# Kernel tuning notes

Measured on AMD Instinct MI355X. Metric: run time of the kernel, lower is better.

Reference implementation:

```python
import jax, jax.numpy as jnp
import numpy as np

N_NODES = 50000
IN_DIM = 128
OUT_DIM = 128
N_EDGES = 800000


def setup_inputs() -> dict:
    key = jax.random.key(0)
    k1, k2, k3, k4 = jax.random.split(key, 4)
    h = jax.random.normal(k1, (N_NODES, IN_DIM), dtype=jnp.float32)
    edges = jax.random.randint(k2, (2, N_EDGES), 0, N_NODES, dtype=jnp.int64)
    # nn.Linear params
    lim = 1.0 / np.sqrt(IN_DIM)
    W = jax.random.uniform(k3, (OUT_DIM, IN_DIM), minval=-lim, maxval=lim, dtype=jnp.float32)
    b = jax.random.uniform(k4, (OUT_DIM,), minval=-lim, maxval=lim, dtype=jnp.float32)
    return {"h": h, "W": W, "b": b, "edges": edges}


def reference(h, W, b, edges):
    n = h.shape[0]
    # add self loops (use_self_loops=True)
    loops = jnp.arange(n, dtype=edges.dtype)
    src = jnp.concatenate([edges[0], loops])  # [E+N]
    dst = jnp.concatenate([edges[1], loops])  # [E+N]
    # linear transform
    h_ = h @ W.T + b  # [N, out_dim]
    # symmetric normalization: 1/sqrt(deg(src)*deg(dst)), degrees incl. self loops
    deg = jax.ops.segment_sum(jnp.ones_like(dst, dtype=h.dtype), dst, num_segments=n)
    ew = jax.lax.rsqrt(deg[src] * deg[dst])  # [E+N]
    # edge-weighted scatter-sum aggregation
    agg = jax.ops.segment_sum(h_[src] * ew[:, None], dst, num_segments=n)
    return agg
```

## Files before the change

### kernel.cpp

```cpp
#include <hip/hip_runtime.h>


#define IN_DIM 128
#define OUT_DIM 128
#define CAP 40
#define NB_A 256
#define NBIN 784
#define BINW 64
#define CAPA 16
#define OVB 8
#define OVCAP 4096

typedef short bf16x8 __attribute__((ext_vector_type(8)));
typedef float f32x4 __attribute__((ext_vector_type(4)));
typedef unsigned short us8 __attribute__((ext_vector_type(8)));
typedef unsigned short us4 __attribute__((ext_vector_type(4)));

__device__ __forceinline__ unsigned short f2bf(float f) {
    unsigned u = __float_as_uint(f);
    u += 0x7fffu + ((u >> 16) & 1u);
    return (unsigned short)(u >> 16);
}
__device__ __forceinline__ float bf2f(unsigned short s) {
    return __uint_as_float(((unsigned)s) << 16);
}
__device__ __forceinline__ void accw(float4& acc, ushort4 v, float wt) {
    acc.x += wt * bf2f(v.x);
    acc.y += wt * bf2f(v.y);
    acc.z += wt * bf2f(v.z);
    acc.w += wt * bf2f(v.w);
}
__device__ __forceinline__ bf16x8 load_a8(const float* h, int row, int k0, int n) {
    bf16x8 r;
    if (row < n) {
        const float4* p = (const float4*)(h + (size_t)row * 128 + k0);
        float4 f0 = p[0], f1 = p[1];
        r[0] = (short)f2bf(f0.x); r[1] = (short)f2bf(f0.y);
        r[2] = (short)f2bf(f0.z); r[3] = (short)f2bf(f0.w);
        r[4] = (short)f2bf(f1.x); r[5] = (short)f2bf(f1.y);
        r[6] = (short)f2bf(f1.z); r[7] = (short)f2bf(f1.w);
    } else {
        r = (bf16x8){0, 0, 0, 0, 0, 0, 0, 0};
    }
    return r;
}

__global__ __launch_bounds__(256) void k_gb(
        const float* __restrict__ h, const float* __restrict__ W,
        const float* __restrict__ b, unsigned short* __restrict__ hsb, int n,
        const int* __restrict__ ed, unsigned* __restrict__ gbuf,
        int* __restrict__ gcnt, int* __restrict__ aovb, int2* __restrict__ aov,
        int* __restrict__ ctrs, int E, int ngemm) {
    __shared__ __align__(16) unsigned short sB[128 * 136];
    __shared__ int ovc;
    __shared__ int2 ovl[OVB];
    const int tid = threadIdx.x;

    if ((int)blockIdx.x >= ngemm) {
        int blk = blockIdx.x - ngemm;
        if (blk == 0 && tid == 0) ctrs[0] = 0;
        int* bc = (int*)sB;
        for (int i = tid; i < NBIN; i += 256) bc[i] = 0;
        if (tid == 0) ovc = 0;
        __syncthreads();
        const int chunk = (E + NB_A - 1) / NB_A;
        const int e0 = blk * chunk, e1 = min(E, e0 + chunk);
        for (int e = e0 + tid; e < e1; e += 256) {
            int s = ed[e];
            int d = ed[E + e];
            int bin = d >> 6, dlo = d & 63;
            int r = atomicAdd(&bc[bin], 1);
            if (r < CAPA) {
                gbuf[((size_t)blk * NBIN + bin) * CAPA + r] =
                    (unsigned)s | ((unsigned)dlo << 16);
            } else {
                int k = atomicAdd(&ovc, 1);
                if (k < OVB) ovl[k] = make_int2(s, d);
            }
        }
        __syncthreads();
        for (int i = tid; i < NBIN; i += 256)
            gcnt[(size_t)blk * NBIN + i] = min(bc[i], CAPA);
        int nov = min(ovc, OVB);
        if (tid < nov) aov[blk * OVB + tid] = ovl[tid];
        if (tid == 0) aovb[blk] = nov;
        return;
    }

    const int lane = tid & 63;
    const int wv = tid >> 6;
    const int quad = lane >> 4;
    const int l16 = lane & 15;
    const int row0 = blockIdx.x * 128;

    {
        const float4* W4 = (const float4*)W;
        for (int t = tid; t < 128 * 32; t += 256) {
            float4 w = W4[t];
            ushort4 q;
            q.x = f2bf(w.x); q.y = f2bf(w.y); q.z = f2bf(w.z); q.w = f2bf(w.w);
            ((ushort4*)sB)[(t >> 5) * 34 + (t & 31)] = q;
        }
    }
    __syncthreads();

    f32x4 acc[2][8];
#pragma unroll
    for (int mt = 0; mt < 2; ++mt)
#pragma unroll
        for (int nt = 0; nt < 8; ++nt) acc[mt][nt] = (f32x4){0.f, 0.f, 0.f, 0.f};

    const int koff = quad * 8;
    const int ra0 = row0 + wv * 32 + l16;
    const int ra1 = ra0 + 16;
#pragma unroll
    for (int kc = 0; kc < 4; ++kc) {
        int kbase = kc * 32 + koff;
        bf16x8 a0 = load_a8(h, ra0, kbase, n);
        bf16x8 a1 = load_a8(h, ra1, kbase, n);
#pragma unroll
        for (int nt = 0; nt < 8; ++nt) {
            bf16x8 bb = *(const bf16x8*)(sB + (nt * 16 + l16) * 136 + kbase);
            acc[0][nt] = __builtin_amdgcn_mfma_f32_16x16x32_bf16(a0, bb, acc[0][nt], 0, 0, 0);
            acc[1][nt] = __builtin_amdgcn_mfma_f32_16x16x32_bf16(a1, bb, acc[1][nt], 0, 0, 0);
        }
    }

#pragma unroll
    for (int mt = 0; mt < 2; ++mt) {
#pragma unroll
        for (int r = 0; r < 4; ++r) {
            int row = row0 + wv * 32 + mt * 16 + quad * 4 + r;
            if (row >= n) continue;
#pragma unroll
            for (int nt = 0; nt < 8; ++nt) {
                int col = nt * 16 + l16;
                hsb[(size_t)row * 128 + col] = f2bf(acc[mt][nt][r] + b[col]);
            }
        }
    }
}

__global__ __launch_bounds__(256) void k_binB(const unsigned* __restrict__ gbuf,
                                              const int* __restrict__ gcnt,
                                              const int* __restrict__ aovb,
                                              const int2* __restrict__ aov,
                                              unsigned short* __restrict__ ell,
                                              int* __restrict__ cnt,
                                              float* __restrict__ rs,
                                              int2* __restrict__ ovf2,
                                              int* __restrict__ ovf2c, int n) {
    __shared__ int lcnt[BINW];
    __shared__ __align__(16) unsigned short ells[BINW * CAP];
    const int tid = threadIdx.x;
    const int bin = blockIdx.x;
    const int node0 = bin * BINW;

    if (tid < BINW) lcnt[tid] = 0;
    __syncthreads();

    {
        int c = gcnt[(size_t)tid * NBIN + bin];
        const int4* cell4 = (const int4*)(gbuf + ((size_t)tid * NBIN + bin) * CAPA);
        int4 q0 = cell4[0];
        int4 q1 = cell4[1];
        int4 q2 = cell4[2];
        int4 q3 = cell4[3];
#define PROC(REC, J)                                              \
        if ((J) < c) {                                            \
            unsigned rec = (unsigned)(REC);                       \
            int src = rec & 0xffff;                               \
            int dlo = rec >> 16;                                  \
            int r = atomicAdd(&lcnt[dlo], 1);                     \
            if (r < CAP) {                                        \
                ells[dlo * CAP + r] = (unsigned short)src;        \
            } else {                                              \
                int k = atomicAdd(ovf2c, 1);                      \
                if (k < OVCAP) ovf2[k] = make_int2(src, node0 + dlo); \
            }                                                     \
        }
        PROC(q0.x, 0)  PROC(q0.y, 1)  PROC(q0.z, 2)  PROC(q0.w, 3)
        PROC(q1.x, 4)  PROC(q1.y, 5)  PROC(q1.z, 6)  PROC(q1.w, 7)
        PROC(q2.x, 8)  PROC(q2.y, 9)  PROC(q2.z, 10) PROC(q2.w, 11)
        PROC(q3.x, 12) PROC(q3.y, 13) PROC(q3.z, 14) PROC(q3.w, 15)
#undef PROC
    }
    {
        int cov = aovb[tid];
        for (int j = 0; j < cov; ++j) {
            int2 p = aov[tid * OVB + j];
            if ((p.y >> 6) == bin) {
                int dlo = p.y & 63;
                int r = atomicAdd(&lcnt[dlo], 1);
                if (r < CAP) {
                    ells[dlo * CAP + r] = (unsigned short)p.x;
                } else {
                    int k = atomicAdd(ovf2c, 1);
                    if (k < OVCAP) ovf2[k] = make_int2(p.x, node0 + dlo);
                }
            }
        }
    }
    __syncthreads();
    if (tid < BINW) {
        int node = node0 + tid;
        if (node < n) {
            cnt[node] = lcnt[tid];
            rs[node] = rsqrtf((float)(lcnt[tid] + 1));
        }
    }
    const int4* sp = (const int4*)ells;
    int4* dp = (int4*)(ell + (size_t)node0 * CAP);
#pragma unroll
    for (int i = tid; i < BINW * CAP * 2 / 16; i += 256) dp[i] = sp[i];
}

__global__ __launch_bounds__(256) void k_agg(const int* __restrict__ cnt,
                                             const float* __restrict__ rs,
                                             const unsigned short* __restrict__ ell,
                                             const int2* __restrict__ ovf2,
                                             const int* __restrict__ ovf2c,
                                             const unsigned short* __restrict__ hsb,
                                             float* __restrict__ out, int n) {
    int node = blockIdx.x * 8 + (threadIdx.x >> 5);
    if (node >= n) return;
    int lane = threadIdx.x & 31;
    int deg = cnt[node];
    float rsn = rs[node];
    int m = min(deg, CAP);

    const ushort4* hp = (const ushort4*)hsb;
    ushort4 sv = hp[(size_t)node * 32 + lane];
    float4 acc;
    acc.x = rsn * bf2f(sv.x); acc.y = rsn * bf2f(sv.y);
    acc.z = rsn * bf2f(sv.z); acc.w = rsn * bf2f(sv.w);

    const unsigned short* row = ell + (size_t)node * CAP;
    int e = 0;
    for (; e + 8 <= m; e += 8) {
        us8 p = *(const us8*)(row + e);
        float w0 = rs[p[0]], w1 = rs[p[1]], w2 = rs[p[2]], w3 = rs[p[3]];
        float w4 = rs[p[4]], w5 = rs[p[5]], w6 = rs[p[6]], w7 = rs[p[7]];
        ushort4 v0 = hp[(size_t)p[0] * 32 + lane];
        ushort4 v1 = hp[(size_t)p[1] * 32 + lane];
        ushort4 v2 = hp[(size_t)p[2] * 32 + lane];
        ushort4 v3 = hp[(size_t)p[3] * 32 + lane];
        ushort4 v4 = hp[(size_t)p[4] * 32 + lane];
        ushort4 v5 = hp[(size_t)p[5] * 32 + lane];
        ushort4 v6 = hp[(size_t)p[6] * 32 + lane];
        ushort4 v7 = hp[(size_t)p[7] * 32 + lane];
        accw(acc, v0, w0); accw(acc, v1, w1); accw(acc, v2, w2); accw(acc, v3, w3);
        accw(acc, v4, w4); accw(acc, v5, w5); accw(acc, v6, w6); accw(acc, v7, w7);
    }
    if (e + 4 <= m) {
        us4 p = *(const us4*)(row + e);
        float w0 = rs[p[0]], w1 = rs[p[1]], w2 = rs[p[2]], w3 = rs[p[3]];
        ushort4 v0 = hp[(size_t)p[0] * 32 + lane];
        ushort4 v1 = hp[(size_t)p[1] * 32 + lane];
        ushort4 v2 = hp[(size_t)p[2] * 32 + lane];
        ushort4 v3 = hp[(size_t)p[3] * 32 + lane];
        accw(acc, v0, w0); accw(acc, v1, w1); accw(acc, v2, w2); accw(acc, v3, w3);
        e += 4;
    }
    for (; e < m; ++e) {
        int s = row[e];
        accw(acc, hp[(size_t)s * 32 + lane], rs[s]);
    }
    if (deg > CAP) {
        int novf = min(*ovf2c, OVCAP);
        for (int i = 0; i < novf; ++i) {
            int2 p = ovf2[i];
            if (p.y == node) {
                accw(acc, hp[(size_t)p.x * 32 + lane], rs[p.x]);
            }
        }
    }
    acc.x *= rsn; acc.y *= rsn; acc.z *= rsn; acc.w *= rsn;
    ((float4*)out)[(size_t)node * 32 + lane] = acc;
}

extern "C" void kernel_launch(void* const* d_in, const int* in_sizes, int n_in,
                              void* d_out, int out_size, void* d_ws, size_t ws_size,
                              hipStream_t stream) {
    const float* h = (const float*)d_in[0];
    const float* W = (const float*)d_in[1];
    const float* b = (const float*)d_in[2];
    const int* edges = (const int*)d_in[3];

    const int n = in_sizes[0] / IN_DIM;
    const int E = in_sizes[3] / 2;
    const int ngemm = (n + 127) / 128;
    const int nnode_pad = NBIN * BINW;

    size_t o = 0;
    auto carve = [&](size_t elems) {
        size_t cur = o;
        o += (elems + 511) & ~(size_t)511;
        return cur;
    };
    float* ws = (float*)d_ws;
    unsigned short* hsb = (unsigned short*)(ws + carve((size_t)n * 64));
    unsigned* gbuf = (unsigned*)(ws + carve((size_t)NB_A * NBIN * CAPA));
    int* gcnt = (int*)(ws + carve((size_t)NB_A * NBIN));
    int* aovb = (int*)(ws + carve(NB_A));
    int2* aov = (int2*)(ws + carve((size_t)NB_A * OVB * 2));
    int* cnt = (int*)(ws + carve(nnode_pad));
    float* rs = ws + carve(nnode_pad);
    unsigned short* ell = (unsigned short*)(ws + carve((size_t)nnode_pad * CAP / 2));
    int2* ovf2 = (int2*)(ws + carve(OVCAP * 2));
    int* ctrs = (int*)(ws + carve(2));

    float* out = (float*)d_out;

    k_gb<<<ngemm + NB_A, 256, 0, stream>>>(h, W, b, hsb, n, edges, gbuf, gcnt,
                                           aovb, aov, ctrs, E, ngemm);
    k_binB<<<NBIN, 256, 0, stream>>>(gbuf, gcnt, aovb, aov, ell, cnt, rs,
                                     ovf2, ctrs, n);
    k_agg<<<(n + 7) / 8, 256, 0, stream>>>(cnt, rs, ell, ovf2, ctrs, hsb, out, n);
}
```

Baseline: 138.5 us.

## Split fused GEMM/binning kernel into separate launches with LDS-staged A tiles

Separates the combined edge-binning and linear-transform kernel into two kernels, k_binA and k_gemm, so the binning blocks no longer share the GEMM kernel's large LDS allocation and grid. The GEMM now uses 64-row tiles and stages the h rows into shared memory as bf16 before the MFMA loop, instead of each wave loading and converting its A fragments straight from global memory. This adds an extra kernel launch and removes the concurrency between binning and GEMM that the fused launch provided. It also doubles the number of GEMM blocks, each of which redundantly converts the full W matrix.

Result: slower. 142.3 us (+2.7%).

```diff
diff --git a/kernel.cpp b/kernel.cpp
--- a/kernel.cpp
+++ b/kernel.cpp
@@ -30,71 +30,70 @@
     acc.z += wt * bf2f(v.z);
     acc.w += wt * bf2f(v.w);
 }
-__device__ __forceinline__ bf16x8 load_a8(const float* h, int row, int k0, int n) {
-    bf16x8 r;
-    if (row < n) {
-        const float4* p = (const float4*)(h + (size_t)row * 128 + k0);
-        float4 f0 = p[0], f1 = p[1];
-        r[0] = (short)f2bf(f0.x); r[1] = (short)f2bf(f0.y);
-        r[2] = (short)f2bf(f0.z); r[3] = (short)f2bf(f0.w);
-        r[4] = (short)f2bf(f1.x); r[5] = (short)f2bf(f1.y);
-        r[6] = (short)f2bf(f1.z); r[7] = (short)f2bf(f1.w);
-    } else {
-        r = (bf16x8){0, 0, 0, 0, 0, 0, 0, 0};
-    }
-    return r;
-}
-
-__global__ __launch_bounds__(256) void k_gb(
-        const float* __restrict__ h, const float* __restrict__ W,
-        const float* __restrict__ b, unsigned short* __restrict__ hsb, int n,
-        const int* __restrict__ ed, unsigned* __restrict__ gbuf,
-        int* __restrict__ gcnt, int* __restrict__ aovb, int2* __restrict__ aov,
-        int* __restrict__ ctrs, int E, int ngemm) {
-    __shared__ __align__(16) unsigned short sB[128 * 136];
+
+__global__ __launch_bounds__(256) void k_binA(const int* __restrict__ ed,
+                                              unsigned* __restrict__ gbuf,
+                                              int* __restrict__ gcnt,
+                                              int* __restrict__ aovb,
+                                              int2* __restrict__ aov,
+                                              int* __restrict__ ctrs, int E) {
+    __shared__ int bc[NBIN];
     __shared__ int ovc;
     __shared__ int2 ovl[OVB];
     const int tid = threadIdx.x;
-
-    if ((int)blockIdx.x >= ngemm) {
-        int blk = blockIdx.x - ngemm;
-        if (blk == 0 && tid == 0) ctrs[0] = 0;
-        int* bc = (int*)sB;
-        for (int i = tid; i < NBIN; i += 256) bc[i] = 0;
-        if (tid == 0) ovc = 0;
-        __syncthreads();
-        const int chunk = (E + NB_A - 1) / NB_A;
-        const int e0 = blk * chunk, e1 = min(E, e0 + chunk);
-        for (int e = e0 + tid; e < e1; e += 256) {
-            int s = ed[e];
-            int d = ed[E + e];
-            int bin = d >> 6, dlo = d & 63;
-            int r = atomicAdd(&bc[bin], 1);
-            if (r < CAPA) {
-                gbuf[((size_t)blk * NBIN + bin) * CAPA + r] =
-                    (unsigned)s | ((unsigned)dlo << 16);
-            } else {
-                int k = atomicAdd(&ovc, 1);
-                if (k < OVB) ovl[k] = make_int2(s, d);
-            }
-        }
-        __syncthreads();
-        for (int i = tid; i < NBIN; i += 256)
-            gcnt[(size_t)blk * NBIN + i] = min(bc[i], CAPA);
-        int nov = min(ovc, OVB);
-        if (tid < nov) aov[blk * OVB + tid] = ovl[tid];
-        if (tid == 0) aovb[blk] = nov;
-        return;
-    }
-
+    const int blk = blockIdx.x;
+    if (blk == 0 && tid == 0) ctrs[0] = 0;
+    for (int i = tid; i < NBIN; i += 256) bc[i] = 0;
+    if (tid == 0) ovc = 0;
+    __syncthreads();
+    const int chunk = (E + NB_A - 1) / NB_A;
+    const int e0 = blk * chunk, e1 = min(E, e0 + chunk);
+    for (int e = e0 + tid; e < e1; e += 256) {
+        int s = ed[e];
+        int d = ed[E + e];
+        int bin = d >> 6, dlo = d & 63;
+        int r = atomicAdd(&bc[bin], 1);
+        if (r < CAPA) {
+            gbuf[((size_t)blk * NBIN + bin) * CAPA + r] =
+                (unsigned)s | ((unsigned)dlo << 16);
+        } else {
+            int k = atomicAdd(&ovc, 1);
+            if (k < OVB) ovl[k] = make_int2(s, d);
+        }
+    }
+    __syncthreads();
+    for (int i = tid; i < NBIN; i += 256)
+        gcnt[(size_t)blk * NBIN + i] = min(bc[i], CAPA);
+    int nov = min(ovc, OVB);
+    if (tid < nov) aov[blk * OVB + tid] = ovl[tid];
+    if (tid == 0) aovb[blk] = nov;
+}
+
+__global__ __launch_bounds__(256) void k_gemm(
+        const float* __restrict__ h, const float* __restrict__ W,
+        const float* __restrict__ b, unsigned short* __restrict__ hsb, int n) {
+    __shared__ unsigned short sA[64 * 136];
+    __shared__ unsigned short sB[128 * 136];
+
+    const int tid = threadIdx.x;
     const int lane = tid & 63;
     const int wv = tid >> 6;
     const int quad = lane >> 4;
     const int l16 = lane & 15;
-    const int row0 = blockIdx.x * 128;
+    const int row0 = blockIdx.x * 64;
 
     {
+        const float4* h4 = (const float4*)h;
         const float4* W4 = (const float4*)W;
+        for (int t = tid; t < 64 * 32; t += 256) {
+            int r = t >> 5, c4 = t & 31;
+            int row = row0 + r;
+            float4 v = make_float4(0.f, 0.f, 0.f, 0.f);
+            if (row < n) v = h4[(size_t)row * 32 + c4];
+            ushort4 p;
+            p.x = f2bf(v.x); p.y = f2bf(v.y); p.z = f2bf(v.z); p.w = f2bf(v.w);
+            ((ushort4*)sA)[r * 34 + c4] = p;
+        }
         for (int t = tid; t < 128 * 32; t += 256) {
             float4 w = W4[t];
             ushort4 q;
@@ -104,39 +103,30 @@
     }
     __syncthreads();
 
-    f32x4 acc[2][8];
-#pragma unroll
-    for (int mt = 0; mt < 2; ++mt)
-#pragma unroll
-        for (int nt = 0; nt < 8; ++nt) acc[mt][nt] = (f32x4){0.f, 0.f, 0.f, 0.f};
+    f32x4 acc[8];
+#pragma unroll
+    for (int nt = 0; nt < 8; ++nt) acc[nt] = (f32x4){0.f, 0.f, 0.f, 0.f};
 
     const int koff = quad * 8;
-    const int ra0 = row0 + wv * 32 + l16;
-    const int ra1 = ra0 + 16;
 #pragma unroll
     for (int kc = 0; kc < 4; ++kc) {
         int kbase = kc * 32 + koff;
-        bf16x8 a0 = load_a8(h, ra0, kbase, n);
-        bf16x8 a1 = load_a8(h, ra1, kbase, n);
+        bf16x8 a0 = *(const bf16x8*)(sA + (wv * 16 + l16) * 136 + kbase);
 #pragma unroll
         for (int nt = 0; nt < 8; ++nt) {
             bf16x8 bb = *(const bf16x8*)(sB + (nt * 16 + l16) * 136 + kbase);
-            acc[0][nt] = __builtin_amdgcn_mfma_f32_16x16x32_bf16(a0, bb, acc[0][nt], 0, 0, 0);
-            acc[1][nt] = __builtin_amdgcn_mfma_f32_16x16x32_bf16(a1, bb, acc[1][nt], 0, 0, 0);
-        }
-    }
-
-#pragma unroll
-    for (int mt = 0; mt < 2; ++mt) {
-#pragma unroll
-        for (int r = 0; r < 4; ++r) {
-            int row = row0 + wv * 32 + mt * 16 + quad * 4 + r;
-            if (row >= n) continue;
-#pragma unroll
-            for (int nt = 0; nt < 8; ++nt) {
-                int col = nt * 16 + l16;
-                hsb[(size_t)row * 128 + col] = f2bf(acc[mt][nt][r] + b[col]);
-            }
+            acc[nt] = __builtin_amdgcn_mfma_f32_16x16x32_bf16(a0, bb, acc[nt], 0, 0, 0);
+        }
+    }
+
+#pragma unroll
+    for (int r = 0; r < 4; ++r) {
+        int row = row0 + wv * 16 + quad * 4 + r;
+        if (row >= n) continue;
+#pragma unroll
+        for (int nt = 0; nt < 8; ++nt) {
+            int col = nt * 16 + l16;
+            hsb[(size_t)row * 128 + col] = f2bf(acc[nt][r] + b[col]);
         }
     }
 }
@@ -289,7 +279,7 @@
 
     const int n = in_sizes[0] / IN_DIM;
     const int E = in_sizes[3] / 2;
-    const int ngemm = (n + 127) / 128;
+    const int ngemm = (n + 63) / 64;
     const int nnode_pad = NBIN * BINW;
 
     size_t o = 0;
@@ -312,8 +302,8 @@
 
     float* out = (float*)d_out;
 
-    k_gb<<<ngemm + NB_A, 256, 0, stream>>>(h, W, b, hsb, n, edges, gbuf, gcnt,
-                                           aovb, aov, ctrs, E, ngemm);
+    k_binA<<<NB_A, 256, 0, stream>>>(edges, gbuf, gcnt, aovb, aov, ctrs, E);
+    k_gemm<<<ngemm, 256, 0, stream>>>(h, W, b, hsb, n);
     k_binB<<<NBIN, 256, 0, stream>>>(gbuf, gcnt, aovb, aov, ell, cnt, rs,
                                      ovf2, ctrs, n);
     k_agg<<<(n + 7) / 8, 256, 0, stream>>>(cnt, rs, ell, ovf2, ctrs, hsb, out, n);
```

## Split GEMM tiles across binning kernels to overlap GEMM with bin passes

Applied to the files above, without the earlier changes.

Moves the linear-transform GEMM into a shared device function and splits its tiles across two launches. The first half runs alongside the edge bin-A pass and the second half alongside the per-bin ELL build. The aim is to balance work across the two kernels, so GEMM blocks fill idle compute units while the memory/atomic-bound binning runs. The bin kernel now uses the larger GEMM shared-memory footprint, which can lower occupancy for bin blocks. The bin kernel's node<n guard is also removed; this relies on cnt/rs being padded to the bin count.

Result: slower. 142.3 us (+2.7%).

```diff
diff --git a/kernel.cpp b/kernel.cpp
--- a/kernel.cpp
+++ b/kernel.cpp
@@ -45,19 +45,78 @@
     return r;
 }
 
-__global__ __launch_bounds__(256) void k_gb(
+__device__ __forceinline__ void gemm_body(
+        unsigned short* sB, const float* __restrict__ h,
+        const float* __restrict__ W, const float* __restrict__ b,
+        unsigned short* __restrict__ hsb, int n, int tile) {
+    const int tid = threadIdx.x;
+    const int lane = tid & 63;
+    const int wv = tid >> 6;
+    const int quad = lane >> 4;
+    const int l16 = lane & 15;
+    const int row0 = tile * 128;
+
+    {
+        const float4* W4 = (const float4*)W;
+        for (int t = tid; t < 128 * 32; t += 256) {
+            float4 w = W4[t];
+            ushort4 q;
+            q.x = f2bf(w.x); q.y = f2bf(w.y); q.z = f2bf(w.z); q.w = f2bf(w.w);
+            ((ushort4*)sB)[(t >> 5) * 34 + (t & 31)] = q;
+        }
+    }
+    __syncthreads();
+
+    f32x4 acc[2][8];
+#pragma unroll
+    for (int mt = 0; mt < 2; ++mt)
+#pragma unroll
+        for (int nt = 0; nt < 8; ++nt) acc[mt][nt] = (f32x4){0.f, 0.f, 0.f, 0.f};
+
+    const int koff = quad * 8;
+    const int ra0 = row0 + wv * 32 + l16;
+    const int ra1 = ra0 + 16;
+#pragma unroll
+    for (int kc = 0; kc < 4; ++kc) {
+        int kbase = kc * 32 + koff;
+        bf16x8 a0 = load_a8(h, ra0, kbase, n);
+        bf16x8 a1 = load_a8(h, ra1, kbase, n);
+#pragma unroll
+        for (int nt = 0; nt < 8; ++nt) {
+            bf16x8 bb = *(const bf16x8*)(sB + (nt * 16 + l16) * 136 + kbase);
+            acc[0][nt] = __builtin_amdgcn_mfma_f32_16x16x32_bf16(a0, bb, acc[0][nt], 0, 0, 0);
+            acc[1][nt] = __builtin_amdgcn_mfma_f32_16x16x32_bf16(a1, bb, acc[1][nt], 0, 0, 0);
+        }
+    }
+
+#pragma unroll
+    for (int mt = 0; mt < 2; ++mt) {
+#pragma unroll
+        for (int r = 0; r < 4; ++r) {
+            int row = row0 + wv * 32 + mt * 16 + quad * 4 + r;
+            if (row >= n) continue;
+#pragma unroll
+            for (int nt = 0; nt < 8; ++nt) {
+                int col = nt * 16 + l16;
+                hsb[(size_t)row * 128 + col] = f2bf(acc[mt][nt][r] + b[col]);
+            }
+        }
+    }
+}
+
+__global__ __launch_bounds__(256) void k_gb1(
         const float* __restrict__ h, const float* __restrict__ W,
         const float* __restrict__ b, unsigned short* __restrict__ hsb, int n,
         const int* __restrict__ ed, unsigned* __restrict__ gbuf,
         int* __restrict__ gcnt, int* __restrict__ aovb, int2* __restrict__ aov,
-        int* __restrict__ ctrs, int E, int ngemm) {
+        int* __restrict__ ctrs, int E, int ng1) {
     __shared__ __align__(16) unsigned short sB[128 * 136];
     __shared__ int ovc;
     __shared__ int2 ovl[OVB];
     const int tid = threadIdx.x;
 
-    if ((int)blockIdx.x >= ngemm) {
-        int blk = blockIdx.x - ngemm;
+    if ((int)blockIdx.x >= ng1) {
+        int blk = blockIdx.x - ng1;
         if (blk == 0 && tid == 0) ctrs[0] = 0;
         int* bc = (int*)sB;
         for (int i = tid; i < NBIN; i += 256) bc[i] = 0;
@@ -86,133 +145,84 @@
         if (tid == 0) aovb[blk] = nov;
         return;
     }
-
-    const int lane = tid & 63;
-    const int wv = tid >> 6;
-    const int quad = lane >> 4;
-    const int l16 = lane & 15;
-    const int row0 = blockIdx.x * 128;
-
-    {
-        const float4* W4 = (const float4*)W;
-        for (int t = tid; t < 128 * 32; t += 256) {
-            float4 w = W4[t];
-            ushort4 q;
-            q.x = f2bf(w.x); q.y = f2bf(w.y); q.z = f2bf(w.z); q.w = f2bf(w.w);
-            ((ushort4*)sB)[(t >> 5) * 34 + (t & 31)] = q;
-        }
-    }
-    __syncthreads();
-
-    f32x4 acc[2][8];
-#pragma unroll
-    for (int mt = 0; mt < 2; ++mt)
-#pragma unroll
-        for (int nt = 0; nt < 8; ++nt) acc[mt][nt] = (f32x4){0.f, 0.f, 0.f, 0.f};
-
-    const int koff = quad * 8;
-    const int ra0 = row0 + wv * 32 + l16;
-    const int ra1 = ra0 + 16;
-#pragma unroll
-    for (int kc = 0; kc < 4; ++kc) {
-        int kbase = kc * 32 + koff;
-        bf16x8 a0 = load_a8(h, ra0, kbase, n);
-        bf16x8 a1 = load_a8(h, ra1, kbase, n);
-#pragma unroll
-        for (int nt = 0; nt < 8; ++nt) {
-            bf16x8 bb = *(const bf16x8*)(sB + (nt * 16 + l16) * 136 + kbase);
-            acc[0][nt] = __builtin_amdgcn_mfma_f32_16x16x32_bf16(a0, bb, acc[0][nt], 0, 0, 0);
-            acc[1][nt] = __builtin_amdgcn_mfma_f32_16x16x32_bf16(a1, bb, acc[1][nt], 0, 0, 0);
-        }
-    }
-
-#pragma unroll
-    for (int mt = 0; mt < 2; ++mt) {
-#pragma unroll
-        for (int r = 0; r < 4; ++r) {
-            int row = row0 + wv * 32 + mt * 16 + quad * 4 + r;
-            if (row >= n) continue;
-#pragma unroll
-            for (int nt = 0; nt < 8; ++nt) {
-                int col = nt * 16 + l16;
-                hsb[(size_t)row * 128 + col] = f2bf(acc[mt][nt][r] + b[col]);
-            }
-        }
-    }
-}
-
-__global__ __launch_bounds__(256) void k_binB(const unsigned* __restrict__ gbuf,
-                                              const int* __restrict__ gcnt,
-                                              const int* __restrict__ aovb,
-                                              const int2* __restrict__ aov,
-                                              unsigned short* __restrict__ ell,
-                                              int* __restrict__ cnt,
-                                              float* __restrict__ rs,
-                                              int2* __restrict__ ovf2,
-                                              int* __restrict__ ovf2c, int n) {
-    __shared__ int lcnt[BINW];
-    __shared__ __align__(16) unsigned short ells[BINW * CAP];
+    gemm_body(sB, h, W, b, hsb, n, blockIdx.x);
+}
+
+__global__ __launch_bounds__(256) void k_gb2(
+        const float* __restrict__ h, const float* __restrict__ W,
+        const float* __restrict__ b, unsigned short* __restrict__ hsb, int n,
+        const unsigned* __restrict__ gbuf, const int* __restrict__ gcnt,
+        const int* __restrict__ aovb, const int2* __restrict__ aov,
+        unsigned short* __restrict__ ell, int* __restrict__ cnt,
+        float* __restrict__ rs, int2* __restrict__ ovf2,
+        int* __restrict__ ovf2c, int tile0, int ng2) {
+    __shared__ __align__(16) unsigned short sB[128 * 136];
     const int tid = threadIdx.x;
-    const int bin = blockIdx.x;
-    const int node0 = bin * BINW;
-
-    if (tid < BINW) lcnt[tid] = 0;
-    __syncthreads();
-
-    {
-        int c = gcnt[(size_t)tid * NBIN + bin];
-        const int4* cell4 = (const int4*)(gbuf + ((size_t)tid * NBIN + bin) * CAPA);
-        int4 q0 = cell4[0];
-        int4 q1 = cell4[1];
-        int4 q2 = cell4[2];
-        int4 q3 = cell4[3];
+
+    if ((int)blockIdx.x >= ng2) {
+        const int bin = blockIdx.x - ng2;
+        const int node0 = bin * BINW;
+        int* lcnt = (int*)sB;
+        unsigned short* ells = sB + 128;
+
+        if (tid < BINW) lcnt[tid] = 0;
+        __syncthreads();
+
+        {
+            int c = gcnt[(size_t)tid * NBIN + bin];
+            const int4* cell4 = (const int4*)(gbuf + ((size_t)tid * NBIN + bin) * CAPA);
+            int4 q0 = cell4[0];
+            int4 q1 = cell4[1];
+            int4 q2 = cell4[2];
+            int4 q3 = cell4[3];
 #define PROC(REC, J)                                              \
-        if ((J) < c) {                                            \
-            unsigned rec = (unsigned)(REC);                       \
-            int src = rec & 0xffff;                               \
-            int dlo = rec >> 16;                                  \
-            int r = atomicAdd(&lcnt[dlo], 1);                     \
-            if (r < CAP) {                                        \
-                ells[dlo * CAP + r] = (unsigned short)src;        \
-            } else {                                              \
-                int k = atomicAdd(ovf2c, 1);                      \
-                if (k < OVCAP) ovf2[k] = make_int2(src, node0 + dlo); \
-            }                                                     \
-        }
-        PROC(q0.x, 0)  PROC(q0.y, 1)  PROC(q0.z, 2)  PROC(q0.w, 3)
-        PROC(q1.x, 4)  PROC(q1.y, 5)  PROC(q1.z, 6)  PROC(q1.w, 7)
-        PROC(q2.x, 8)  PROC(q2.y, 9)  PROC(q2.z, 10) PROC(q2.w, 11)
-        PROC(q3.x, 12) PROC(q3.y, 13) PROC(q3.z, 14) PROC(q3.w, 15)
+            if ((J) < c) {                                        \
+                unsigned rec = (unsigned)(REC);                   \
+                int src = rec & 0xffff;                           \
+                int dlo = rec >> 16;                              \
+                int r = atomicAdd(&lcnt[dlo], 1);                 \
+                if (r < CAP) {                                    \
+                    ells[dlo * CAP + r] = (unsigned short)src;    \
+                } else {                                          \
+                    int k = atomicAdd(ovf2c, 1);                  \
+                    if (k < OVCAP) ovf2[k] = make_int2(src, node0 + dlo); \
+                }                                                 \
+            }
+            PROC(q0.x, 0)  PROC(q0.y, 1)  PROC(q0.z, 2)  PROC(q0.w, 3)
+            PROC(q1.x, 4)  PROC(q1.y, 5)  PROC(q1.z, 6)  PROC(q1.w, 7)
+            PROC(q2.x, 8)  PROC(q2.y, 9)  PROC(q2.z, 10) PROC(q2.w, 11)
+            PROC(q3.x, 12) PROC(q3.y, 13) PROC(q3.z, 14) PROC(q3.w, 15)
 #undef PROC
-    }
-    {
-        int cov = aovb[tid];
-        for (int j = 0; j < cov; ++j) {
-            int2 p = aov[tid * OVB + j];
-            if ((p.y >> 6) == bin) {
-                int dlo = p.y & 63;
-                int r = atomicAdd(&lcnt[dlo], 1);
-                if (r < CAP) {
-                    ells[dlo * CAP + r] = (unsigned short)p.x;
-                } else {
-                    int k = atomicAdd(ovf2c, 1);
-                    if (k < OVCAP) ovf2[k] = make_int2(p.x, node0 + dlo);
+        }
+        {
+            int cov = aovb[tid];
+            for (int j = 0; j < cov; ++j) {
+                int2 p = aov[tid * OVB + j];
+                if ((p.y >> 6) == bin) {
+                    int dlo = p.y & 63;
+                    int r = atomicAdd(&lcnt[dlo], 1);
+                    if (r < CAP) {
+                        ells[dlo * CAP + r] = (unsigned short)p.x;
+                    } else {
+                        int k = atomicAdd(ovf2c, 1);
+                        if (k < OVCAP) ovf2[k] = make_int2(p.x, node0 + dlo);
+                    }
                 }
             }
         }
-    }
-    __syncthreads();
-    if (tid < BINW) {
-        int node = node0 + tid;
-        if (node < n) {
+        __syncthreads();
+        if (tid < BINW) {
+            int node = node0 + tid;
             cnt[node] = lcnt[tid];
             rs[node] = rsqrtf((float)(lcnt[tid] + 1));
         }
-    }
-    const int4* sp = (const int4*)ells;
-    int4* dp = (int4*)(ell + (size_t)node0 * CAP);
-#pragma unroll
-    for (int i = tid; i < BINW * CAP * 2 / 16; i += 256) dp[i] = sp[i];
+        const int4* sp = (const int4*)ells;
+        int4* dp = (int4*)(ell + (size_t)node0 * CAP);
+#pragma unroll
+        for (int i = tid; i < BINW * CAP * 2 / 16; i += 256) dp[i] = sp[i];
+        return;
+    }
+    gemm_body(sB, h, W, b, hsb, n, tile0 + blockIdx.x);
 }
 
 __global__ __launch_bounds__(256) void k_agg(const int* __restrict__ cnt,
@@ -290,6 +300,8 @@
     const int n = in_sizes[0] / IN_DIM;
     const int E = in_sizes[3] / 2;
     const int ngemm = (n + 127) / 128;
+    const int ng1 = (ngemm + 1) / 2;
+    const int ng2 = ngemm - ng1;
     const int nnode_pad = NBIN * BINW;
 
     size_t o = 0;
@@ -312,9 +324,10 @@
 
     float* out = (float*)d_out;
 
-    k_gb<<<ngemm + NB_A, 256, 0, stream>>>(h, W, b, hsb, n, edges, gbuf, gcnt,
-                                           aovb, aov, ctrs, E, ngemm);
-    k_binB<<<NBIN, 256, 0, stream>>>(gbuf, gcnt, aovb, aov, ell, cnt, rs,
-                                     ovf2, ctrs, n);
+    k_gb1<<<ng1 + NB_A, 256, 0, stream>>>(h, W, b, hsb, n, edges, gbuf, gcnt,
+                                          aovb, aov, ctrs, E, ng1);
+    k_gb2<<<ng2 + NBIN, 256, 0, stream>>>(h, W, b, hsb, n, gbuf, gcnt, aovb,
+                                          aov, ell, cnt, rs, ovf2, ctrs,
+                                          ng1, ng2);
     k_agg<<<(n + 7) / 8, 256, 0, stream>>>(cnt, rs, ell, ovf2, ctrs, hsb, out, n);
 }
```
